# Performance work log

Measured on AMD Instinct MI355X. Metric: run time of the kernel, lower is better.

Reference implementation:

```python
import jax, jax.numpy as jnp
import numpy as np

IN_DIM = 128
OUT_DIM = 128
NUM_HEADS = 4
HEAD_DIM = OUT_DIM // NUM_HEADS  # 32
B, N = 4, 4096


def setup_inputs() -> dict:
    key = jax.random.key(0)
    ks = jax.random.split(key, 7)
    s_in = 1.0 / np.sqrt(IN_DIM)
    s_out = 1.0 / np.sqrt(OUT_DIM)
    return {
        "x": jax.random.normal(ks[0], (B, N, IN_DIM), dtype=jnp.float32),
        "adjacency": jax.random.randint(ks[1], (N, N), 0, 2, dtype=jnp.int32),
        "W_q": jax.random.uniform(ks[2], (IN_DIM, NUM_HEADS * HEAD_DIM), jnp.float32, -s_in, s_in),
        "W_k": jax.random.uniform(ks[3], (IN_DIM, NUM_HEADS * HEAD_DIM), jnp.float32, -s_in, s_in),
        "W_v": jax.random.uniform(ks[4], (IN_DIM, NUM_HEADS * HEAD_DIM), jnp.float32, -s_in, s_in),
        "W_o": jax.random.uniform(ks[5], (OUT_DIM, OUT_DIM), jnp.float32, -s_out, s_out),
        "b_o": jax.random.uniform(ks[6], (OUT_DIM,), jnp.float32, -s_out, s_out),
    }


def reference(x, adjacency, W_q, W_k, W_v, W_o, b_o):
    Bn, Nn, _ = x.shape
    # QKV projections -> (B, H, N, Dh)
    q = (x @ W_q).reshape(Bn, Nn, NUM_HEADS, HEAD_DIM).transpose(0, 2, 1, 3)
    k = (x @ W_k).reshape(Bn, Nn, NUM_HEADS, HEAD_DIM).transpose(0, 2, 1, 3)
    v = (x @ W_v).reshape(Bn, Nn, NUM_HEADS, HEAD_DIM).transpose(0, 2, 1, 3)
    scores = jnp.einsum("bhnd,bhmd->bhnm", q, k) / np.sqrt(HEAD_DIM).astype(np.float32)
    # adjacency mask (1,1,N,N): -inf where no edge
    adj = adjacency[None, None, :, :]
    scores = jnp.where(adj == 0, -jnp.inf, scores)
    attn = jax.nn.softmax(scores, axis=-1)
    out = jnp.einsum("bhnm,bhmd->bhnd", attn, v)
    out = out.transpose(0, 2, 1, 3).reshape(Bn, Nn, NUM_HEADS * HEAD_DIM)  # concat heads
    return out @ W_o + b_o
```

## Files before the change

kernel.cpp:

```cpp
#include <hip/hip_runtime.h>
#include <stdint.h>

typedef __attribute__((ext_vector_type(4))) short short4v;
typedef __attribute__((ext_vector_type(8))) short bf16x8;
typedef __attribute__((ext_vector_type(4))) float f32x4;
typedef __attribute__((ext_vector_type(2))) uint32_t uint2v;
typedef __attribute__((ext_vector_type(4))) uint32_t uint4v;
typedef __attribute__((ext_vector_type(4))) uint16_t ushort4v;

#define NN 4096

__device__ __forceinline__ uint16_t f2bf(float f) {
    union { float f; uint32_t u; } c; c.f = f;
    uint32_t r = c.u + 0x7FFF + ((c.u >> 16) & 1);
    return (uint16_t)(r >> 16);
}

__global__ __launch_bounds__(256) void wpack_kernel(
    const float* __restrict__ Wq, const float* __restrict__ Wk,
    const float* __restrict__ Wv, const float* __restrict__ Wo,
    uint16_t* __restrict__ WT, uint16_t* __restrict__ WoT)
{
    const int t = blockIdx.x * 256 + threadIdx.x;
    if (t < 3 * 128 * 128) {
        int j = t >> 7, k = t & 127;
        int m = j >> 7, jj = j & 127;
        const float* W = (m == 0) ? Wq : ((m == 1) ? Wk : Wv);
        float v = W[k * 128 + jj];
        if (m == 0) v *= (0.17677669529663687f * 1.4426950408889634f);
        WT[t] = f2bf(v);
    } else {
        int t2 = t - 3 * 128 * 128;
        int j = t2 >> 7, k = t2 & 127;
        WoT[t2] = f2bf(Wo[k * 128 + j]);
    }
}

__global__ __launch_bounds__(256) void adjqkv_kernel(
    const int* __restrict__ adj, uint32_t* __restrict__ bitsT32,
    const float* __restrict__ x, const uint16_t* __restrict__ WT,
    uint16_t* __restrict__ Q, uint16_t* __restrict__ Kf, uint16_t* __restrict__ Vf)
{
    const int blk = blockIdx.x;
    const int tid = threadIdx.x;
    const int wave = tid >> 6, lane = tid & 63;

    if (blk >= 768) {
        const int ablk = blk - 768;
        const int wid = (ablk * 256 + tid) >> 6;
        const int base = wid * 32;
        const int row = base >> 6;
        const int w64b = base & 63;
        const int* src = adj + (size_t)base * 64 + lane;
#pragma unroll 1
        for (int ii = 0; ii < 32; ii += 4) {
            int v0 = src[(ii + 0) * 64];
            int v1 = src[(ii + 1) * 64];
            int v2 = src[(ii + 2) * 64];
            int v3 = src[(ii + 3) * 64];
            uint64_t m0 = __ballot(v0 != 0);
            uint64_t m1 = __ballot(v1 != 0);
            uint64_t m2 = __ballot(v2 != 0);
            uint64_t m3 = __ballot(v3 != 0);
            if (lane == 0) {
                const int w0 = (w64b + ii) * 2;
                bitsT32[(size_t)(w0 + 0) * 4096 + row] = (uint32_t)m0;
                bitsT32[(size_t)(w0 + 1) * 4096 + row] = (uint32_t)(m0 >> 32);
                bitsT32[(size_t)(w0 + 2) * 4096 + row] = (uint32_t)m1;
                bitsT32[(size_t)(w0 + 3) * 4096 + row] = (uint32_t)(m1 >> 32);
                bitsT32[(size_t)(w0 + 4) * 4096 + row] = (uint32_t)m2;
                bitsT32[(size_t)(w0 + 5) * 4096 + row] = (uint32_t)(m2 >> 32);
                bitsT32[(size_t)(w0 + 6) * 4096 + row] = (uint32_t)m3;
                bitsT32[(size_t)(w0 + 7) * 4096 + row] = (uint32_t)(m3 >> 32);
            }
        }
        return;
    }

    const int g = lane >> 4, l15 = lane & 15;
    const int m = blk >> 8;
    const int ntile = (blk & 255) * 4 + wave;
    const int n = ntile * 16 + l15;
    const int b = n >> 12, nn = n & 4095;

    const char* xrow = (const char*)x + (size_t)n * 512;
    bf16x8 xb[4];
#pragma unroll
    for (int ks = 0; ks < 4; ++ks) {
        f32x4 a = *(const f32x4*)(xrow + ks * 128 + g * 16);
        f32x4 c = *(const f32x4*)(xrow + ks * 128 + 64 + g * 16);
        bf16x8 f;
#pragma unroll
        for (int i = 0; i < 4; ++i) { f[i] = (short)f2bf(a[i]); f[4 + i] = (short)f2bf(c[i]); }
        xb[ks] = f;
    }

#pragma unroll 1
    for (int jt = m * 8; jt < m * 8 + 8; ++jt) {
        const int j0 = jt * 16;
        const bool isV = (m == 2);
        const char* wrow = (const char*)WT + (size_t)(j0 + l15) * 256;
        f32x4 acc = {0.f, 0.f, 0.f, 0.f};
#pragma unroll
        for (int ks = 0; ks < 4; ++ks) {
            short4v a0 = *(const short4v*)(wrow + ks * 64 + g * 8);
            short4v a1 = *(const short4v*)(wrow + ks * 64 + 32 + g * 8);
            bf16x8 af = __builtin_shufflevector(a0, a1, 0, 1, 2, 3, 4, 5, 6, 7);
            acc = isV ? __builtin_amdgcn_mfma_f32_16x16x32_bf16(xb[ks], af, acc, 0, 0, 0)
                      : __builtin_amdgcn_mfma_f32_16x16x32_bf16(af, xb[ks], acc, 0, 0, 0);
        }
        const int bh = b * 4 + ((j0 & 127) >> 5);
        const int half = (j0 >> 4) & 1;
        ushort4v st;
#pragma unroll
        for (int r = 0; r < 4; ++r) st[r] = f2bf(acc[r]);
        if (m == 0) {
            const int d0 = (j0 & 31) + g * 4;
            *(ushort4v*)(Q + ((size_t)bh * 4096 + nn) * 32 + d0) = st;
        } else if (m == 1) {
            *(ushort4v*)(Kf + ((size_t)bh << 17) + (ntile & 255) * 512 + lane * 8 + half * 4) = st;
        } else {
            *(ushort4v*)(Vf + ((size_t)bh << 17) + ((ntile & 255) >> 1) * 1024
                         + half * 512 + lane * 8 + ((ntile & 1) << 2)) = st;
        }
    }
}

__global__ __launch_bounds__(256) void attn_kernel(
    const uint16_t* __restrict__ Q, const uint16_t* __restrict__ Kf,
    const uint16_t* __restrict__ Vf, const uint32_t* __restrict__ bitsT32,
    uint16_t* __restrict__ O)
{
    __shared__ f32x4 cmb[4][4][2][64];
    __shared__ float csum[4][4][64];
    const int tid = threadIdx.x;
    const int wave = tid >> 6, lane = tid & 63;
    const int g = lane >> 4, l15 = lane & 15, gsh = g * 4;
    const int blk = blockIdx.x;
    const int bh = ((blk & 7) << 1) | ((blk >> 3) & 1);
    const int qb = blk >> 4;
    const int q0 = qb * 64;

    const char* Kbase = (const char*)Kf + ((size_t)bh << 18) + wave * 65536 + lane * 16;
    const char* Vbase = (const char*)Vf + ((size_t)bh << 18) + wave * 65536 + lane * 16;
    const uint32_t* mb[4];
#pragma unroll
    for (int qg = 0; qg < 4; ++qg)
        mb[qg] = bitsT32 + (size_t)(wave * 32) * 4096 + (q0 + qg * 16 + l15);

    bf16x8 qf[4];
#pragma unroll
    for (int qg = 0; qg < 4; ++qg) {
        const char* qrow = (const char*)Q + ((size_t)bh * 4096 + q0 + qg * 16 + l15) * 64;
        short4v a0 = *(const short4v*)(qrow + g * 8);
        short4v a1 = *(const short4v*)(qrow + 32 + g * 8);
        qf[qg] = __builtin_shufflevector(a0, a1, 0, 1, 2, 3, 4, 5, 6, 7);
    }

    bf16x8 ones;
#pragma unroll
    for (int i = 0; i < 8; ++i) ones[i] = (short)0x3F80;

    const f32x4 z = {0.f, 0.f, 0.f, 0.f};
    f32x4 o[4][2], sacc[4];
#pragma unroll
    for (int qg = 0; qg < 4; ++qg) { o[qg][0] = z; o[qg][1] = z; sacc[qg] = z; }

    bf16x8 kc[4], kn[4];
    uint2v wc[4], wn[4];
#pragma unroll
    for (int j = 0; j < 4; ++j) kc[j] = *(const bf16x8*)(Kbase + j * 1024);
#pragma unroll
    for (int qg = 0; qg < 4; ++qg) {
        wc[qg][0] = mb[qg][0];
        wc[qg][1] = mb[qg][4096];
    }

    auto body = [&](int tcur, int tnxt, bf16x8 (&kcur)[4], uint2v (&wcur)[4],
                    bf16x8 (&knxt)[4], uint2v (&wnxt)[4]) {
        if (tnxt < 16) {
#pragma unroll
            for (int j = 0; j < 4; ++j)
                knxt[j] = *(const bf16x8*)(Kbase + (size_t)tnxt * 4096 + j * 1024);
#pragma unroll
            for (int qg = 0; qg < 4; ++qg) {
                wnxt[qg][0] = mb[qg][(size_t)(2 * tnxt) * 4096];
                wnxt[qg][1] = mb[qg][(size_t)(2 * tnxt + 1) * 4096];
            }
        }
        bf16x8 vc[4];
#pragma unroll
        for (int i = 0; i < 4; ++i)
            vc[i] = *(const bf16x8*)(Vbase + (size_t)tcur * 4096 + i * 1024);

#pragma unroll
        for (int qg = 0; qg < 4; ++qg) {
            f32x4 s[4];
#pragma unroll
            for (int j = 0; j < 4; ++j)
                s[j] = __builtin_amdgcn_mfma_f32_16x16x32_bf16(kcur[j], qf[qg], z, 0, 0, 0);
            float p[16];
#pragma unroll
            for (int j = 0; j < 4; ++j) {
                uint32_t wj = wcur[qg][j >> 1] >> (((j & 1) << 4) + gsh);
#pragma unroll
                for (int r = 0; r < 4; ++r) {
                    float pv = __builtin_amdgcn_exp2f(s[j][r]);
                    int msk = ((int)(wj << (31 - r))) >> 31;
                    p[j * 4 + r] = __uint_as_float(__float_as_uint(pv) & (uint32_t)msk);
                }
            }
            uint32_t pk[8];
#pragma unroll
            for (int i = 0; i < 8; ++i) {
                uint32_t r_;
                asm("v_cvt_pk_bf16_f32 %0, %1, %2" : "=v"(r_) : "v"(p[2 * i]), "v"(p[2 * i + 1]));
                pk[i] = r_;
            }
            uint4v u0 = {pk[0], pk[1], pk[2], pk[3]};
            uint4v u1 = {pk[4], pk[5], pk[6], pk[7]};
            bf16x8 pf0 = __builtin_bit_cast(bf16x8, u0);
            bf16x8 pf1 = __builtin_bit_cast(bf16x8, u1);
            o[qg][0] = __builtin_amdgcn_mfma_f32_16x16x32_bf16(vc[0], pf0, o[qg][0], 0, 0, 0);
            o[qg][0] = __builtin_amdgcn_mfma_f32_16x16x32_bf16(vc[2], pf1, o[qg][0], 0, 0, 0);
            o[qg][1] = __builtin_amdgcn_mfma_f32_16x16x32_bf16(vc[1], pf0, o[qg][1], 0, 0, 0);
            o[qg][1] = __builtin_amdgcn_mfma_f32_16x16x32_bf16(vc[3], pf1, o[qg][1], 0, 0, 0);
            sacc[qg] = __builtin_amdgcn_mfma_f32_16x16x32_bf16(ones, pf0, sacc[qg], 0, 0, 0);
            sacc[qg] = __builtin_amdgcn_mfma_f32_16x16x32_bf16(ones, pf1, sacc[qg], 0, 0, 0);
        }
    };

#pragma unroll 1
    for (int tt = 0; tt < 16; tt += 2) {
        body(tt, tt + 1, kc, wc, kn, wn);
        body(tt + 1, tt + 2, kn, wn, kc, wc);
    }

#pragma unroll
    for (int qg = 0; qg < 4; ++qg) {
        cmb[wave][qg][0][lane] = o[qg][0];
        cmb[wave][qg][1][lane] = o[qg][1];
        csum[wave][qg][lane] = sacc[qg][0];
    }
    __syncthreads();
    {
        const int qg = wave;
        f32x4 a0 = cmb[0][qg][0][lane];
        f32x4 a1 = cmb[0][qg][1][lane];
        float sd = csum[0][qg][lane];
#pragma unroll
        for (int v = 1; v < 4; ++v) {
            a0 += cmb[v][qg][0][lane];
            a1 += cmb[v][qg][1][lane];
            sd += csum[v][qg][lane];
        }
        const float inv = 1.0f / sd;
        const int q = q0 + qg * 16 + l15;
        uint16_t* orow = O + ((size_t)bh * 4096 + q) * 32;
        ushort4v st0, st1;
#pragma unroll
        for (int r = 0; r < 4; ++r) {
            st0[r] = f2bf(a0[r] * inv);
            st1[r] = f2bf(a1[r] * inv);
        }
        *(ushort4v*)(orow + gsh) = st0;
        *(ushort4v*)(orow + 16 + gsh) = st1;
    }
}

__global__ __launch_bounds__(256) void proj_kernel(
    const uint16_t* __restrict__ A, const uint16_t* __restrict__ WoT,
    const float* __restrict__ bo, float* __restrict__ out)
{
    const int wave = threadIdx.x >> 6, lane = threadIdx.x & 63;
    const int g = lane >> 4, l15 = lane & 15;
    const int blk = blockIdx.x;
    const int ctbase = (blk >> 8) * 2;
    const int ntile = (blk & 255) * 4 + wave;
    const int n = ntile * 16 + l15;
    const int b = n >> 12, nn = n & 4095;

    bf16x8 bfr[4];
#pragma unroll
    for (int h = 0; h < 4; ++h) {
        const char* arow = (const char*)A + (((size_t)(b * 4 + h)) * 4096 + nn) * 64;
        short4v a0 = *(const short4v*)(arow + g * 8);
        short4v a1 = *(const short4v*)(arow + 32 + g * 8);
        bfr[h] = __builtin_shufflevector(a0, a1, 0, 1, 2, 3, 4, 5, 6, 7);
    }
#pragma unroll 1
    for (int ct = ctbase; ct < ctbase + 2; ++ct) {
        const int c0 = ct * 16;
        const char* wrow = (const char*)WoT + (size_t)(c0 + l15) * 256;
        f32x4 acc = {0.f, 0.f, 0.f, 0.f};
#pragma unroll
        for (int h = 0; h < 4; ++h) {
            short4v a0 = *(const short4v*)(wrow + h * 64 + g * 8);
            short4v a1 = *(const short4v*)(wrow + h * 64 + 32 + g * 8);
            bf16x8 af = __builtin_shufflevector(a0, a1, 0, 1, 2, 3, 4, 5, 6, 7);
            acc = __builtin_amdgcn_mfma_f32_16x16x32_bf16(af, bfr[h], acc, 0, 0, 0);
        }
        f32x4 bias = *(const f32x4*)(bo + c0 + g * 4);
#pragma unroll
        for (int r = 0; r < 4; ++r) acc[r] += bias[r];
        *(f32x4*)(out + (size_t)n * 128 + c0 + g * 4) = acc;
    }
}

extern "C" void kernel_launch(void* const* d_in, const int* in_sizes, int n_in,
                              void* d_out, int out_size, void* d_ws, size_t ws_size,
                              hipStream_t stream)
{
    const float* x   = (const float*)d_in[0];
    const int*   adj = (const int*)d_in[1];
    const float* Wq  = (const float*)d_in[2];
    const float* Wk  = (const float*)d_in[3];
    const float* Wv  = (const float*)d_in[4];
    const float* Wo  = (const float*)d_in[5];
    const float* bo  = (const float*)d_in[6];
    float* out = (float*)d_out;

    char* ws = (char*)d_ws;
    uint16_t* Q      = (uint16_t*)(ws);
    uint16_t* Kf     = (uint16_t*)(ws + ((size_t)4 << 20));
    uint16_t* Vf     = (uint16_t*)(ws + ((size_t)8 << 20));
    uint16_t* AO     = (uint16_t*)(ws + ((size_t)12 << 20));
    uint32_t* bitsT32= (uint32_t*)(ws + ((size_t)16 << 20));
    uint16_t* WT     = (uint16_t*)(ws + ((size_t)18 << 20));
    uint16_t* WoT    = (uint16_t*)(ws + ((size_t)18 << 20) + 98304);

    hipLaunchKernelGGL(wpack_kernel, dim3(256), dim3(256), 0, stream,
                       Wq, Wk, Wv, Wo, WT, WoT);
    hipLaunchKernelGGL(adjqkv_kernel, dim3(2816), dim3(256), 0, stream,
                       adj, bitsT32, x, WT, Q, Kf, Vf);
    hipLaunchKernelGGL(attn_kernel, dim3(1024), dim3(256), 0, stream,
                       Q, Kf, Vf, bitsT32, AO);
    hipLaunchKernelGGL(proj_kernel, dim3(1024), dim3(256), 0, stream,
                       AO, WoT, bo, out);
}
```

Measured before the change: 120.8 us.

## Replace MFMA row-sum with VALU accumulation, widen adj-bit unroll, split proj grid

Three separate changes are made. The softmax denominator is now accumulated with scalar adds of the unpacked p values plus cross-lane shuffles, instead of two extra MFMAs against a ones vector per query group, which frees matrix-core cycles in the attention loop. The adjacency bit-packing loop issues 8 loads and ballots per iteration instead of 4, giving more memory-level parallelism. The projection kernel gives each block one output column tile instead of two and launches twice as many blocks. The new sum uses fp32 values before bf16 rounding, so it differs slightly from the bf16 P fed to the PV MFMA, and it adds VALU work.

Measured after the change: 126.4 us. 4.7% more time.

```diff
diff --git a/kernel.cpp b/kernel.cpp
--- a/kernel.cpp
+++ b/kernel.cpp
@@ -53,25 +53,20 @@
         const int w64b = base & 63;
         const int* src = adj + (size_t)base * 64 + lane;
 #pragma unroll 1
-        for (int ii = 0; ii < 32; ii += 4) {
-            int v0 = src[(ii + 0) * 64];
-            int v1 = src[(ii + 1) * 64];
-            int v2 = src[(ii + 2) * 64];
-            int v3 = src[(ii + 3) * 64];
-            uint64_t m0 = __ballot(v0 != 0);
-            uint64_t m1 = __ballot(v1 != 0);
-            uint64_t m2 = __ballot(v2 != 0);
-            uint64_t m3 = __ballot(v3 != 0);
+        for (int ii = 0; ii < 32; ii += 8) {
+            int v[8];
+#pragma unroll
+            for (int k = 0; k < 8; ++k) v[k] = src[(ii + k) * 64];
+            uint64_t m[8];
+#pragma unroll
+            for (int k = 0; k < 8; ++k) m[k] = __ballot(v[k] != 0);
             if (lane == 0) {
                 const int w0 = (w64b + ii) * 2;
-                bitsT32[(size_t)(w0 + 0) * 4096 + row] = (uint32_t)m0;
-                bitsT32[(size_t)(w0 + 1) * 4096 + row] = (uint32_t)(m0 >> 32);
-                bitsT32[(size_t)(w0 + 2) * 4096 + row] = (uint32_t)m1;
-                bitsT32[(size_t)(w0 + 3) * 4096 + row] = (uint32_t)(m1 >> 32);
-                bitsT32[(size_t)(w0 + 4) * 4096 + row] = (uint32_t)m2;
-                bitsT32[(size_t)(w0 + 5) * 4096 + row] = (uint32_t)(m2 >> 32);
-                bitsT32[(size_t)(w0 + 6) * 4096 + row] = (uint32_t)m3;
-                bitsT32[(size_t)(w0 + 7) * 4096 + row] = (uint32_t)(m3 >> 32);
+#pragma unroll
+                for (int k = 0; k < 8; ++k) {
+                    bitsT32[(size_t)(w0 + 2 * k + 0) * 4096 + row] = (uint32_t)m[k];
+                    bitsT32[(size_t)(w0 + 2 * k + 1) * 4096 + row] = (uint32_t)(m[k] >> 32);
+                }
             }
         }
         return;
@@ -157,14 +152,11 @@
         qf[qg] = __builtin_shufflevector(a0, a1, 0, 1, 2, 3, 4, 5, 6, 7);
     }
 
-    bf16x8 ones;
-#pragma unroll
-    for (int i = 0; i < 8; ++i) ones[i] = (short)0x3F80;
-
     const f32x4 z = {0.f, 0.f, 0.f, 0.f};
-    f32x4 o[4][2], sacc[4];
-#pragma unroll
-    for (int qg = 0; qg < 4; ++qg) { o[qg][0] = z; o[qg][1] = z; sacc[qg] = z; }
+    f32x4 o[4][2];
+    float srun[4];
+#pragma unroll
+    for (int qg = 0; qg < 4; ++qg) { o[qg][0] = z; o[qg][1] = z; srun[qg] = 0.f; }
 
     bf16x8 kc[4], kn[4];
     uint2v wc[4], wn[4];
@@ -210,6 +202,11 @@
                     p[j * 4 + r] = __uint_as_float(__float_as_uint(pv) & (uint32_t)msk);
                 }
             }
+            float ps = 0.f;
+#pragma unroll
+            for (int i = 0; i < 16; ++i) ps += p[i];
+            srun[qg] += ps;
+
             uint32_t pk[8];
 #pragma unroll
             for (int i = 0; i < 8; ++i) {
@@ -225,8 +222,6 @@
             o[qg][0] = __builtin_amdgcn_mfma_f32_16x16x32_bf16(vc[2], pf1, o[qg][0], 0, 0, 0);
             o[qg][1] = __builtin_amdgcn_mfma_f32_16x16x32_bf16(vc[1], pf0, o[qg][1], 0, 0, 0);
             o[qg][1] = __builtin_amdgcn_mfma_f32_16x16x32_bf16(vc[3], pf1, o[qg][1], 0, 0, 0);
-            sacc[qg] = __builtin_amdgcn_mfma_f32_16x16x32_bf16(ones, pf0, sacc[qg], 0, 0, 0);
-            sacc[qg] = __builtin_amdgcn_mfma_f32_16x16x32_bf16(ones, pf1, sacc[qg], 0, 0, 0);
         }
     };
 
@@ -238,9 +233,11 @@
 
 #pragma unroll
     for (int qg = 0; qg < 4; ++qg) {
+        srun[qg] += __shfl_xor(srun[qg], 16);
+        srun[qg] += __shfl_xor(srun[qg], 32);
         cmb[wave][qg][0][lane] = o[qg][0];
         cmb[wave][qg][1][lane] = o[qg][1];
-        csum[wave][qg][lane] = sacc[qg][0];
+        csum[wave][qg][lane] = srun[qg];
     }
     __syncthreads();
     {
@@ -275,7 +272,7 @@
     const int wave = threadIdx.x >> 6, lane = threadIdx.x & 63;
     const int g = lane >> 4, l15 = lane & 15;
     const int blk = blockIdx.x;
-    const int ctbase = (blk >> 8) * 2;
+    const int ct = blk >> 8;
     const int ntile = (blk & 255) * 4 + wave;
     const int n = ntile * 16 + l15;
     const int b = n >> 12, nn = n & 4095;
@@ -288,8 +285,7 @@
         short4v a1 = *(const short4v*)(arow + 32 + g * 8);
         bfr[h] = __builtin_shufflevector(a0, a1, 0, 1, 2, 3, 4, 5, 6, 7);
     }
-#pragma unroll 1
-    for (int ct = ctbase; ct < ctbase + 2; ++ct) {
+    {
         const int c0 = ct * 16;
         const char* wrow = (const char*)WoT + (size_t)(c0 + l15) * 256;
         f32x4 acc = {0.f, 0.f, 0.f, 0.f};
@@ -335,6 +331,6 @@
                        adj, bitsT32, x, WT, Q, Kf, Vf);
     hipLaunchKernelGGL(attn_kernel, dim3(1024), dim3(256), 0, stream,
                        Q, Kf, Vf, bitsT32, AO);
-    hipLaunchKernelGGL(proj_kernel, dim3(1024), dim3(256), 0, stream,
+    hipLaunchKernelGGL(proj_kernel, dim3(2048), dim3(256), 0, stream,
                        AO, WoT, bo, out);
 }
```
